# Kernel optimization log

Hardware: AMD Instinct MI355X
Metric: run time of the kernel (lower is better)

## Reference

```python
import jax, jax.numpy as jnp
import numpy as np


def _elu_feature_map(x):
    return jax.nn.elu(x) + 1.0


def setup_inputs() -> dict:
    key = jax.random.key(0)
    kq, kk, kv = jax.random.split(key, 3)
    shape = (4, 4096, 8, 64)  # n, s, h, d
    Q = jax.random.normal(kq, shape, dtype=jnp.float32)
    K = jax.random.normal(kk, shape, dtype=jnp.float32)
    V = jax.random.normal(kv, shape, dtype=jnp.float32)
    return {"Q": Q, "K": K, "V": V}


def reference(Q, K, V):
    eps = 1e-06
    Qf = _elu_feature_map(Q)  # [n,l,h,d]
    Kf = _elu_feature_map(K)  # [n,s,h,d]
    v_length = V.shape[1]
    Vn = V / v_length  # normalize values for numerical stability
    # KV: [n,h,d,v] -- sum over sequence of K outer V
    KV = jnp.einsum('nshd,nshv->nhdv', Kf, Vn)
    # Z: inverse normalizer [n,l,h]
    Z = 1.0 / (jnp.einsum('nlhd,nhd->nlh', Qf, Kf.sum(axis=1)) + eps)
    out = jnp.einsum('nlhd,nhdv,nlh->nlhv', Qf, KV, Z) * v_length
    return out
```

## Files before the change

### kernel.cpp

```cpp
#include <hip/hip_runtime.h>
#include <math.h>

#define SEQ 4096
#define NH  8
#define DIM 64

__device__ __forceinline__ float elu1(float x) {
    return x > 0.0f ? x + 1.0f : __expf(x);
}

__global__ __launch_bounds__(256) void k_phase1(const float* __restrict__ Kin,
                                                const float* __restrict__ Vin,
                                                float* __restrict__ pKV,
                                                float* __restrict__ pKs,
                                                int NC, int sLen) {
    const int nh = blockIdx.x / NC;
    const int ck = blockIdx.x % NC;
    const int n  = nh >> 3, h = nh & 7;
    const int t  = threadIdx.x;
    const int r  = t >> 4;
    const int c  = (t & 15) * 4;
    const int d0 = (t >> 4) * 4;
    const int v0 = (t & 15) * 4;

    __shared__ __align__(16) float kf[2][16][64];
    __shared__ __align__(16) float vv[2][16][64];

    float acc[4][4];
#pragma unroll
    for (int i = 0; i < 4; i++)
#pragma unroll
        for (int j = 0; j < 4; j++) acc[i][j] = 0.0f;
    float ks[4] = {0.0f, 0.0f, 0.0f, 0.0f};

    const int s0 = ck * sLen;
    const int iters = sLen >> 4;

    {
        const size_t g = ((size_t)(n * SEQ + s0 + r) * NH + h) * DIM + c;
        float4 k4 = *(const float4*)(Kin + g);
        float4 v4 = *(const float4*)(Vin + g);
        float4 f4;
        f4.x = elu1(k4.x); f4.y = elu1(k4.y); f4.z = elu1(k4.z); f4.w = elu1(k4.w);
        ks[0] += f4.x; ks[1] += f4.y; ks[2] += f4.z; ks[3] += f4.w;
        *(float4*)&kf[0][r][c] = f4;
        *(float4*)&vv[0][r][c] = v4;
    }

    for (int it = 0; it < iters; ++it) {
        __syncthreads();
        const int cur = it & 1;
        float4 k4, v4;
        const bool more = (it + 1 < iters);
        if (more) {
            const size_t g = ((size_t)(n * SEQ + s0 + (it + 1) * 16 + r) * NH + h) * DIM + c;
            k4 = *(const float4*)(Kin + g);
            v4 = *(const float4*)(Vin + g);
        }
#pragma unroll
        for (int ss = 0; ss < 16; ++ss) {
            float4 a4 = *(const float4*)&kf[cur][ss][d0];
            float4 b4 = *(const float4*)&vv[cur][ss][v0];
            float a[4] = {a4.x, a4.y, a4.z, a4.w};
            float b[4] = {b4.x, b4.y, b4.z, b4.w};
#pragma unroll
            for (int i = 0; i < 4; i++)
#pragma unroll
                for (int j = 0; j < 4; j++)
                    acc[i][j] = fmaf(a[i], b[j], acc[i][j]);
        }
        if (more) {
            float4 f4;
            f4.x = elu1(k4.x); f4.y = elu1(k4.y); f4.z = elu1(k4.z); f4.w = elu1(k4.w);
            ks[0] += f4.x; ks[1] += f4.y; ks[2] += f4.z; ks[3] += f4.w;
            *(float4*)&kf[cur ^ 1][r][c] = f4;
            *(float4*)&vv[cur ^ 1][r][c] = v4;
        }
    }

    float* dst = pKV + ((size_t)ck * 32 + nh) * 4096;
#pragma unroll
    for (int i = 0; i < 4; i++) {
        float4 o;
        o.x = acc[i][0]; o.y = acc[i][1]; o.z = acc[i][2]; o.w = acc[i][3];
        *(float4*)(dst + (d0 + i) * 64 + v0) = o;
    }

    __syncthreads();
    *(float4*)&kf[0][r][c] = make_float4(ks[0], ks[1], ks[2], ks[3]);
    __syncthreads();
    if (t < 64) {
        float s = 0.0f;
#pragma unroll
        for (int rr = 0; rr < 16; ++rr) s += kf[0][rr][t];
        pKs[((size_t)ck * 32 + nh) * 64 + t] = s;
    }
}

template <int NC>
__global__ __launch_bounds__(128) void k_reduceT(const float* __restrict__ pKV,
                                                 const float* __restrict__ pKs,
                                                 float* __restrict__ KVf,
                                                 float* __restrict__ Ksf) {
    const int gid = blockIdx.x * 128 + threadIdx.x;
    const float4* p4 = (const float4*)pKV;
    float4 s = make_float4(0.f, 0.f, 0.f, 0.f);
#pragma unroll
    for (int c = 0; c < NC; ++c) {
        float4 v = p4[(size_t)c * 32768 + gid];
        s.x += v.x; s.y += v.y; s.z += v.z; s.w += v.w;
    }
    ((float4*)KVf)[gid] = s;
    if (gid < 2048) {
        float ss = 0.0f;
#pragma unroll
        for (int c = 0; c < NC; ++c) ss += pKs[(size_t)c * 2048 + gid];
        Ksf[gid] = ss;
    }
}

__global__ __launch_bounds__(128) void k_reduceG(const float* __restrict__ pKV,
                                                 const float* __restrict__ pKs,
                                                 float* __restrict__ KVf,
                                                 float* __restrict__ Ksf, int NC) {
    const int gid = blockIdx.x * 128 + threadIdx.x;
    const float4* p4 = (const float4*)pKV;
    float4 s = make_float4(0.f, 0.f, 0.f, 0.f);
    for (int c = 0; c < NC; ++c) {
        float4 v = p4[(size_t)c * 32768 + gid];
        s.x += v.x; s.y += v.y; s.z += v.z; s.w += v.w;
    }
    ((float4*)KVf)[gid] = s;
    if (gid < 2048) {
        float ss = 0.0f;
        for (int c = 0; c < NC; ++c) ss += pKs[(size_t)c * 2048 + gid];
        Ksf[gid] = ss;
    }
}

__global__ __launch_bounds__(256) void k_phase2(const float* __restrict__ Qin,
                                                const float* __restrict__ KVf,
                                                const float* __restrict__ Ksf,
                                                float* __restrict__ Out) {
    const int nh   = blockIdx.x >> 4;
    const int tile = blockIdx.x & 15;
    const int n = nh >> 3, h = nh & 7;
    const int t = threadIdx.x;

    __shared__ __align__(16) float Qt[32 * 256];
    __shared__ __align__(16) float KVs[64][64];
    __shared__ float Kss[64];

    {
        const float4* src = (const float4*)(KVf + (size_t)nh * 4096);
        float4* dst = (float4*)&KVs[0][0];
#pragma unroll
        for (int i = 0; i < 4; ++i) dst[t + 256 * i] = src[t + 256 * i];
        if (t < 64) Kss[t] = Ksf[nh * 64 + t];
    }

    const int l0 = tile * 256;
    const int r0 = (t >> 3) * 8;
    const int v0 = (t & 7) * 8;

    float acc[8][8];
#pragma unroll
    for (int i = 0; i < 8; i++)
#pragma unroll
        for (int j = 0; j < 8; j++) acc[i][j] = 0.0f;
    float p[8] = {0.f, 0.f, 0.f, 0.f, 0.f, 0.f, 0.f, 0.f};

    for (int dc = 0; dc < 2; ++dc) {
        if (dc) __syncthreads();
#pragma unroll
        for (int i = 0; i < 8; ++i) {
            const int j   = t + 256 * i;
            const int row = j >> 3;
            const int dl4 = (j & 7) << 2;
            const size_t g = ((size_t)(n * SEQ + l0 + row) * NH + h) * DIM + dc * 32 + dl4;
            float4 q4 = *(const float4*)(Qin + g);
            const int col = row ^ dl4;
            Qt[(dl4 + 0) * 256 + col] = elu1(q4.x);
            Qt[(dl4 + 1) * 256 + col] = elu1(q4.y);
            Qt[(dl4 + 2) * 256 + col] = elu1(q4.z);
            Qt[(dl4 + 3) * 256 + col] = elu1(q4.w);
        }
        __syncthreads();

#pragma unroll 2
        for (int dl = 0; dl < 32; ++dl) {
            const int d = dc * 32 + dl;
            const int s = dl & ~3;
            float4 qa = *(const float4*)&Qt[dl * 256 + (r0 ^ s)];
            float4 qb = *(const float4*)&Qt[dl * 256 + ((r0 + 4) ^ s)];
            float4 ka = *(const float4*)&KVs[d][v0];
            float4 kb = *(const float4*)&KVs[d][v0 + 4];
            const float ksd = Kss[d];
            float q[8]  = {qa.x, qa.y, qa.z, qa.w, qb.x, qb.y, qb.z, qb.w};
            float kv[8] = {ka.x, ka.y, ka.z, ka.w, kb.x, kb.y, kb.z, kb.w};
#pragma unroll
            for (int i = 0; i < 8; ++i) {
                p[i] = fmaf(q[i], ksd, p[i]);
#pragma unroll
                for (int jj = 0; jj < 8; ++jj)
                    acc[i][jj] = fmaf(q[i], kv[jj], acc[i][jj]);
            }
        }
    }

#pragma unroll
    for (int i = 0; i < 8; ++i) {
        const float z = 1.0f / (p[i] + 1e-6f);
        const int l = l0 + r0 + i;
        float* o = Out + ((size_t)(n * SEQ + l) * NH + h) * DIM + v0;
        float4 oa, ob;
        oa.x = acc[i][0] * z; oa.y = acc[i][1] * z; oa.z = acc[i][2] * z; oa.w = acc[i][3] * z;
        ob.x = acc[i][4] * z; ob.y = acc[i][5] * z; ob.z = acc[i][6] * z; ob.w = acc[i][7] * z;
        *(float4*)(o)     = oa;
        *(float4*)(o + 4) = ob;
    }
}

extern "C" void kernel_launch(void* const* d_in, const int* in_sizes, int n_in,
                              void* d_out, int out_size, void* d_ws, size_t ws_size,
                              hipStream_t stream) {
    const float* Q = (const float*)d_in[0];
    const float* K = (const float*)d_in[1];
    const float* V = (const float*)d_in[2];
    float* out = (float*)d_out;

    int NC = 32;
    const size_t unit = 133120ull * 4ull;
    while (NC > 1 && (size_t)(NC + 1) * unit > ws_size) NC >>= 1;
    const int sLen = SEQ / NC;

    float* KVf = (float*)d_ws;
    float* Ksf = KVf + 32 * 4096;
    float* pKV = Ksf + 32 * 64;
    float* pKs = pKV + (size_t)NC * 32 * 4096;

    hipLaunchKernelGGL(k_phase1, dim3(32 * NC), dim3(256), 0, stream, K, V, pKV, pKs, NC, sLen);
    switch (NC) {
        case 32: hipLaunchKernelGGL(k_reduceT<32>, dim3(256), dim3(128), 0, stream, pKV, pKs, KVf, Ksf); break;
        case 16: hipLaunchKernelGGL(k_reduceT<16>, dim3(256), dim3(128), 0, stream, pKV, pKs, KVf, Ksf); break;
        case 8:  hipLaunchKernelGGL(k_reduceT<8>,  dim3(256), dim3(128), 0, stream, pKV, pKs, KVf, Ksf); break;
        default: hipLaunchKernelGGL(k_reduceG, dim3(256), dim3(128), 0, stream, pKV, pKs, KVf, Ksf, NC); break;
    }
    hipLaunchKernelGGL(k_phase2, dim3(512), dim3(256), 0, stream, Q, KVf, Ksf, out);
}
```

Baseline: 56.78 us.

## Use 8x8 register tiles with wave-split sequence reduction in KV phase

Phase 1 now has each wavefront accumulate a full 64x64 KV tile with 8x8 per-thread register blocking over a quarter of the sequence rows. The four partial tiles are then summed through a 16KB shared buffer, which raises FMA-to-LDS-load ratio but adds a serialized cross-wave reduction and more registers. Chunk count drops from 32 to 16, so partial writes and reduce traffic shrink while per-block work grows. Phase 2 shrinks its Q staging tile to 16 dims per pass, cutting shared memory at the cost of more barriers.

```diff
diff --git a/kernel.cpp b/kernel.cpp
--- a/kernel.cpp
+++ b/kernel.cpp
@@ -20,17 +20,20 @@
     const int t  = threadIdx.x;
     const int r  = t >> 4;
     const int c  = (t & 15) * 4;
-    const int d0 = (t >> 4) * 4;
-    const int v0 = (t & 15) * 4;
+    const int wv   = t >> 6;
+    const int lane = t & 63;
+    const int d0 = (lane >> 3) * 8;
+    const int v0 = (lane & 7) * 8;
 
     __shared__ __align__(16) float kf[2][16][64];
     __shared__ __align__(16) float vv[2][16][64];
-
-    float acc[4][4];
-#pragma unroll
-    for (int i = 0; i < 4; i++)
-#pragma unroll
-        for (int j = 0; j < 4; j++) acc[i][j] = 0.0f;
+    __shared__ __align__(16) float sred[4096];
+
+    float acc[8][8];
+#pragma unroll
+    for (int i = 0; i < 8; i++)
+#pragma unroll
+        for (int j = 0; j < 8; j++) acc[i][j] = 0.0f;
     float ks[4] = {0.0f, 0.0f, 0.0f, 0.0f};
 
     const int s0 = ck * sLen;
@@ -58,15 +61,18 @@
             v4 = *(const float4*)(Vin + g);
         }
 #pragma unroll
-        for (int ss = 0; ss < 16; ++ss) {
-            float4 a4 = *(const float4*)&kf[cur][ss][d0];
-            float4 b4 = *(const float4*)&vv[cur][ss][v0];
-            float a[4] = {a4.x, a4.y, a4.z, a4.w};
-            float b[4] = {b4.x, b4.y, b4.z, b4.w};
-#pragma unroll
-            for (int i = 0; i < 4; i++)
-#pragma unroll
-                for (int j = 0; j < 4; j++)
+        for (int ssi = 0; ssi < 4; ++ssi) {
+            const int ss = wv * 4 + ssi;
+            float4 a0 = *(const float4*)&kf[cur][ss][d0];
+            float4 a1 = *(const float4*)&kf[cur][ss][d0 + 4];
+            float4 b0 = *(const float4*)&vv[cur][ss][v0];
+            float4 b1 = *(const float4*)&vv[cur][ss][v0 + 4];
+            float a[8] = {a0.x, a0.y, a0.z, a0.w, a1.x, a1.y, a1.z, a1.w};
+            float b[8] = {b0.x, b0.y, b0.z, b0.w, b1.x, b1.y, b1.z, b1.w};
+#pragma unroll
+            for (int i = 0; i < 8; i++)
+#pragma unroll
+                for (int j = 0; j < 8; j++)
                     acc[i][j] = fmaf(a[i], b[j], acc[i][j]);
         }
         if (more) {
@@ -78,12 +84,34 @@
         }
     }
 
-    float* dst = pKV + ((size_t)ck * 32 + nh) * 4096;
-#pragma unroll
-    for (int i = 0; i < 4; i++) {
-        float4 o;
-        o.x = acc[i][0]; o.y = acc[i][1]; o.z = acc[i][2]; o.w = acc[i][3];
-        *(float4*)(dst + (d0 + i) * 64 + v0) = o;
+#pragma unroll
+    for (int src = 3; src >= 1; --src) {
+        __syncthreads();
+        if (wv == src) {
+#pragma unroll
+            for (int i = 0; i < 8; i++)
+#pragma unroll
+                for (int j = 0; j < 8; j++) sred[(i * 8 + j) * 64 + lane] = acc[i][j];
+        }
+        __syncthreads();
+        if (wv == src - 1) {
+#pragma unroll
+            for (int i = 0; i < 8; i++)
+#pragma unroll
+                for (int j = 0; j < 8; j++) acc[i][j] += sred[(i * 8 + j) * 64 + lane];
+        }
+    }
+
+    if (wv == 0) {
+        float* dst = pKV + ((size_t)ck * 32 + nh) * 4096;
+#pragma unroll
+        for (int i = 0; i < 8; i++) {
+            float4 oa, ob;
+            oa.x = acc[i][0]; oa.y = acc[i][1]; oa.z = acc[i][2]; oa.w = acc[i][3];
+            ob.x = acc[i][4]; ob.y = acc[i][5]; ob.z = acc[i][6]; ob.w = acc[i][7];
+            *(float4*)(dst + (d0 + i) * 64 + v0)     = oa;
+            *(float4*)(dst + (d0 + i) * 64 + v0 + 4) = ob;
+        }
     }
 
     __syncthreads();
@@ -147,7 +175,7 @@
     const int n = nh >> 3, h = nh & 7;
     const int t = threadIdx.x;
 
-    __shared__ __align__(16) float Qt[32 * 256];
+    __shared__ __align__(16) float Qt[16 * 256];
     __shared__ __align__(16) float KVs[64][64];
     __shared__ float Kss[64];
 
@@ -170,14 +198,14 @@
         for (int j = 0; j < 8; j++) acc[i][j] = 0.0f;
     float p[8] = {0.f, 0.f, 0.f, 0.f, 0.f, 0.f, 0.f, 0.f};
 
-    for (int dc = 0; dc < 2; ++dc) {
+    for (int dc = 0; dc < 4; ++dc) {
         if (dc) __syncthreads();
 #pragma unroll
-        for (int i = 0; i < 8; ++i) {
+        for (int i = 0; i < 4; ++i) {
             const int j   = t + 256 * i;
-            const int row = j >> 3;
-            const int dl4 = (j & 7) << 2;
-            const size_t g = ((size_t)(n * SEQ + l0 + row) * NH + h) * DIM + dc * 32 + dl4;
+            const int row = j >> 2;
+            const int dl4 = (j & 3) << 2;
+            const size_t g = ((size_t)(n * SEQ + l0 + row) * NH + h) * DIM + dc * 16 + dl4;
             float4 q4 = *(const float4*)(Qin + g);
             const int col = row ^ dl4;
             Qt[(dl4 + 0) * 256 + col] = elu1(q4.x);
@@ -188,9 +216,9 @@
         __syncthreads();
 
 #pragma unroll 2
-        for (int dl = 0; dl < 32; ++dl) {
-            const int d = dc * 32 + dl;
-            const int s = dl & ~3;
+        for (int dl = 0; dl < 16; ++dl) {
+            const int d = dc * 16 + dl;
+            const int s = dl & 12;
             float4 qa = *(const float4*)&Qt[dl * 256 + (r0 ^ s)];
             float4 qb = *(const float4*)&Qt[dl * 256 + ((r0 + 4) ^ s)];
             float4 ka = *(const float4*)&KVs[d][v0];
@@ -229,7 +257,7 @@
     const float* V = (const float*)d_in[2];
     float* out = (float*)d_out;
 
-    int NC = 32;
+    int NC = 16;
     const size_t unit = 133120ull * 4ull;
     while (NC > 1 && (size_t)(NC + 1) * unit > ws_size) NC >>= 1;
     const int sLen = SEQ / NC;
```

New measurement: 55.34 us. -2.5%, faster.
